# Kernel optimization log

Measured on AMD Instinct MI355X. Metric: run time of the kernel, lower is better.

The kernel has to match this reference:

```python
import jax, jax.numpy as jnp
import numpy as np

GAMMA, RHO, OMEGA = 0.7, 2.0, 0.5
EPS = 1e-6


def setup_inputs() -> dict:
    key = jax.random.key(0)
    S, T, N = 64, 256, 1024
    ks = jax.random.split(key, 7)
    x0 = jax.random.normal(ks[0], (N, 1), dtype=jnp.float32)
    # strictly increasing interaction times so dt > 0
    t = jnp.cumsum(jax.random.uniform(ks[1], (S, T), dtype=jnp.float32) + 0.1, axis=1)
    speed = jax.random.uniform(ks[2], (S, 1, 1, 1), dtype=jnp.float32) + 0.1
    vola = jax.random.uniform(ks[3], (S, 1, 1, 1), dtype=jnp.float32) + 0.1
    adj = (jax.random.uniform(ks[4], (N, N)) < 32.0 / N).astype(jnp.float32)
    noise = jax.random.normal(ks[5], (S, T - 1, N, 1), dtype=jnp.float32)
    items = jax.random.randint(ks[6], (S, T), 0, N)
    return {"x0": x0, "t": t, "speed": speed, "vola": vola,
            "adj": adj, "noise": noise, "items": items}


def _simulate(x0, t, speed, vola, adj, noise, items):
    S, T = t.shape
    N = x0.shape[0]
    dt = jnp.diff(t, axis=1)[:, :, None, None]                     # [S,T-1,1,1]
    # OU std: sqrt(vola^2 * (1 - exp(-2*speed*dt)) / (2*speed + 1e-6))
    scale = jnp.sqrt(vola * vola * (1.0 - jnp.exp(-2.0 * speed * dt))
                     / (2.0 * speed + 1e-6))                       # [S,T-1,1,1]
    noisy = noise * scale                                          # [S,T-1,N,1]

    adj_t = adj.T
    in_deg = adj_t.sum(axis=1)[None, :, None]                      # [1,N,1]
    has_in = in_deg > 0

    seq = jnp.arange(S)
    feat0 = jnp.zeros((S, N, 3), jnp.float32)
    feat0 = feat0.at[seq, items[:, 0], 0].add(1.0)
    feat0 = feat0.at[seq, items[:, 0], 2].add(1.0)
    x_init = jnp.broadcast_to(x0[None], (S, N, 1)).astype(jnp.float32)
    sp = speed[:, 0]                                               # [S,1,1]

    def step(carry, inp):
        x_prev, feat = carry
        dt_i, noisy_i, item_i = inp                                # [S,1,1],[S,N,1],[S]
        agg = jnp.einsum('mn,snk->smk', adj_t, x_prev)             # neighbor sum
        empower = jnp.where(has_in, GAMMA * agg / (in_deg + 1e-7), 0.0)
        stable = (feat[..., 1:2] / (feat[..., 0:1] + EPS)) ** RHO
        level = OMEGA * empower + (1.0 - OMEGA) * stable
        e = jnp.exp(-sp * dt_i)
        x_i = x_prev * e + (1.0 - e) * level + noisy_i
        cur_perf = jax.nn.sigmoid(x_i[seq, item_i, 0])
        success = (cur_perf >= 0.5).astype(jnp.float32)
        feat = feat.at[seq, item_i, 0].add(1.0)
        feat = feat.at[seq, item_i, 1].add(success)
        return (x_i, feat), x_i

    xs = (jnp.moveaxis(dt, 1, 0), jnp.moveaxis(noisy, 1, 0), items[:, 1:].T)
    (_, _), ys = jax.lax.scan(step, (x_init, feat0), xs)
    x = jnp.concatenate([x_init[:, None], jnp.moveaxis(ys, 0, 1)], axis=1)  # [S,T,N,1]
    return x


def reference(x0, t, speed, vola, adj, noise, items):
    return _simulate(x0, t, speed, vola, adj, noise, items)
```

## Files before the change

kernel.cpp:

```cpp
#include <hip/hip_runtime.h>

#define NN 1024
#define TT 256
#define MAXDEG 96

typedef unsigned short u16;
typedef unsigned long long ull;


__device__ __forceinline__ int bofsB(int v) {
    int h = (v >> 5) & 31;
    return 1024 + ((v & ~31) | ((v & 31) ^ h));
}
__device__ __forceinline__ int bofsC(int v) {
    int h = (v >> 5) & 31;
    return 2048 + ((v & ~31) | ((v & 31) ^ ((13 * h + 5) & 31)));
}
__device__ __forceinline__ int cnt_res(int pd, int res) {
    return (pd > res) ? (((pd - 1 - res) >> 5) + 1) : 0;
}
__device__ __forceinline__ int pd_of(int deg) {
    int cap = deg < MAXDEG ? deg : MAXDEG;
    int pd = (cap + 15) & ~7;
    if (pd < 16) pd = 16;
    if (pd > MAXDEG) pd = MAXDEG;
    return pd;
}

__global__ __launch_bounds__(64) void k1_count(const float* __restrict__ adj,
                                               int* __restrict__ cnt_part)
{
    int tid = blockIdx.x * 64 + threadIdx.x;
    int chunk = tid >> 10;
    int n = tid & 1023;
    int c = 0;
    for (int j = 0; j < 64; ++j)
        c += (adj[(chunk * 64 + j) * NN + n] != 0.0f) ? 1 : 0;
    cnt_part[chunk * NN + n] = c;
}

__global__ __launch_bounds__(1024) void k23_rank(const int* __restrict__ cnt_part,
                                                 int* __restrict__ deg,
                                                 int* __restrict__ rank_of,
                                                 int* __restrict__ node_of)
{
    __shared__ int pd_s[NN];
    const int n = threadIdx.x;
    int tot = 0;
    for (int c = 0; c < 16; ++c) tot += cnt_part[c * NN + n];
    deg[n] = tot;
    int my = pd_of(tot);
    pd_s[n] = my;
    __syncthreads();
    int r = 0;
    for (int m = 0; m < NN; ++m) {
        int pm = pd_s[m];
        r += (pm > my) || (pm == my && m < n);
    }
    rank_of[n] = r;
    node_of[r] = n;
}

__global__ __launch_bounds__(64) void k4_fill(const float* __restrict__ adj,
                                              const int* __restrict__ cnt_part,
                                              u16* __restrict__ nbrC)
{
    int tid = blockIdx.x * 64 + threadIdx.x;
    int chunk = tid >> 10;
    int n = tid & 1023;
    int pos = 0;
    for (int c = 0; c < chunk; ++c) pos += cnt_part[c * NN + n];
    for (int j = 0; j < 64; ++j) {
        int m = chunk * 64 + j;
        if (adj[m * NN + n] != 0.0f) {
            if (pos < MAXDEG) nbrC[n * MAXDEG + pos] = (u16)m;
            ++pos;
        }
    }
}

__global__ __launch_bounds__(64) void k5_sched(const u16* __restrict__ nbrC,
                                               const int* __restrict__ deg,
                                               const int* __restrict__ rank_of,
                                               u16* __restrict__ nbr8,
                                               int* __restrict__ ngrp_r,
                                               float* __restrict__ invd_r)
{
    const int tl = threadIdx.x;
    const int n  = blockIdx.x * 64 + tl;
    const int r  = rank_of[n];
    const int l  = r & 63;
    const int dg = deg[n];
    const int cap = dg < MAXDEG ? dg : MAXDEG;
    const int pd = pd_of(dg);

    ull freep = 0;
    for (int res = 0; res < 32; ++res)
        freep |= (ull)cnt_res(pd, res) << (2 * res);

    for (int g = 0; g < (pd >> 3); ++g) {
        uint4 pk;
        unsigned w0 = (unsigned)((3072 + ((l + g * 8 + 0) & 31)) * 4);
        unsigned w1 = (unsigned)((3072 + ((l + g * 8 + 1) & 31)) * 4);
        unsigned w2 = (unsigned)((3072 + ((l + g * 8 + 2) & 31)) * 4);
        unsigned w3 = (unsigned)((3072 + ((l + g * 8 + 3) & 31)) * 4);
        unsigned w4 = (unsigned)((3072 + ((l + g * 8 + 4) & 31)) * 4);
        unsigned w5 = (unsigned)((3072 + ((l + g * 8 + 5) & 31)) * 4);
        unsigned w6 = (unsigned)((3072 + ((l + g * 8 + 6) & 31)) * 4);
        unsigned w7 = (unsigned)((3072 + ((l + g * 8 + 7) & 31)) * 4);
        pk.x = w0 | (w1 << 16);
        pk.y = w2 | (w3 << 16);
        pk.z = w4 | (w5 << 16);
        pk.w = w6 | (w7 << 16);
        *(uint4*)(nbr8 + (g << 13) + (r << 3)) = pk;
    }

    const uint4* __restrict__ row = (const uint4*)(nbrC + n * MAXDEG);
    int maxk = 15;

    for (int c8 = 0; c8 < (cap + 7) / 8; ++c8) {
        uint4 w = row[c8];
        int id[8];
        id[0] = w.x & 0xFFFF; id[1] = w.x >> 16;
        id[2] = w.y & 0xFFFF; id[3] = w.y >> 16;
        id[4] = w.z & 0xFFFF; id[5] = w.z >> 16;
        id[6] = w.w & 0xFFFF; id[7] = w.w >> 16;
        int rk[8];
        #pragma unroll
        for (int u = 0; u < 8; ++u)
            rk[u] = rank_of[id[u]];

        int lim = cap - c8 * 8; if (lim > 8) lim = 8;
        #pragma unroll
        for (int u = 0; u < 8; ++u) {
            if (u >= lim) break;
            int v = rk[u];
            int b0 = v & 31;
            int h  = (v >> 5) & 31;
            int b1 = b0 ^ h;
            int b2 = b0 ^ ((13 * h + 5) & 31);
            int res0 = (b0 - l) & 31;
            int res1 = (b1 - l) & 31;
            int res2 = (b2 - l) & 31;
            int f0 = (int)((freep >> (2 * res0)) & 3);
            int f1 = (int)((freep >> (2 * res1)) & 3);
            int f2 = (int)((freep >> (2 * res2)) & 3);
            int kslot = -1, word = v, resw = 0, fw = 0;
            if (f0 > 0 && f0 >= f1 && f0 >= f2) {
                resw = res0; fw = f0; word = v;
            } else if (f1 > 0 && f1 >= f2) {
                resw = res1; fw = f1; word = bofsB(v);
            } else if (f2 > 0) {
                resw = res2; fw = f2; word = bofsC(v);
            } else {
                for (int res = 0; res < 32; ++res) {
                    int f = (int)((freep >> (2 * res)) & 3);
                    if (f > 0) { resw = res; fw = f; word = v; break; }
                }
            }
            if (fw > 0) {
                kslot = resw + 32 * (cnt_res(pd, resw) - fw);
                freep -= 1ull << (2 * resw);
                nbr8[((kslot >> 3) << 13) + (r << 3) + (kslot & 7)] = (u16)(word * 4);
                if (kslot > maxk) maxk = kslot;
            }
        }
    }
    ngrp_r[r] = (maxk >> 3) + 1;
    invd_r[r] = 0.35f / ((float)dg + 1e-7f);
}

#define LDS_BARRIER() asm volatile("s_waitcnt lgkmcnt(0)\n\ts_barrier" ::: "memory")

__global__ __launch_bounds__(1024) void sim_kernel(
    const float* __restrict__ x0, const float* __restrict__ t,
    const float* __restrict__ speed, const float* __restrict__ vola,
    const float* __restrict__ noise, const int* __restrict__ items,
    const u16* __restrict__ nbr8, const int* __restrict__ node_of,
    const int* __restrict__ rank_of,
    const int* __restrict__ ngrp_r, const float* __restrict__ invd_r,
    float* __restrict__ out)
{
    __shared__ float xb[2][3104];
    __shared__ float4 cst[TT - 1];

    const int s   = blockIdx.x;
    const int tid = threadIdx.x;

    const float sp = speed[s];
    const float vo = vola[s];

    if (tid < TT - 1) {
        float t0 = t[s * TT + tid], t1 = t[s * TT + tid + 1];
        float dt = t1 - t0;
        float e  = expf(-sp * dt);
        float sc = vo * sqrtf((1.0f - e * e) / (2.0f * sp + 1e-6f));
        int   it = items[s * TT + tid + 1];
        cst[tid] = make_float4(e, sc, __int_as_float(it), 0.0f);
    }

    const int   m     = node_of[tid];
    const int   r_out = rank_of[tid];
    const int   wB    = bofsB(tid);
    const int   wC    = bofsC(tid);

    const float x0m = x0[m];
    xb[0][tid] = x0m;
    xb[0][wB]  = x0m;
    xb[0][wC]  = x0m;
    if (tid < 32) { xb[0][3072 + tid] = 0.0f; xb[1][3072 + tid] = 0.0f; }

    float* __restrict__ outp = out + (size_t)s * TT * NN + tid;
    outp[0] = x0[tid];

    const int   ng   = ngrp_r[tid];
    const float invd = invd_r[tid];
    const int   item0 = items[s * TT];
    float a_f = (m == item0) ? 1.0f : 0.0f;
    float s_f = 0.0f;

    const float* __restrict__ nzm = noise + (size_t)s * (TT - 1) * NN + m;
    float nzA = nzm[0];
    float nzB = nzm[NN];

    const uint4* __restrict__ nb = (const uint4*)nbr8 + tid;
    uint4 q0  = nb[0];
    uint4 q1  = nb[1024];
    uint4 q2  = nb[2048];
    uint4 q3  = nb[3072];
    uint4 q4  = nb[4096];
    uint4 q5  = nb[5120];
    uint4 q6  = nb[6144];
    uint4 q7  = nb[7168];
    uint4 q8  = nb[8192];
    uint4 q9  = nb[9216];
    uint4 q10 = nb[10240];
    uint4 q11 = nb[11264];

    __syncthreads();

    float x_own = x0m;

#define G8(V)                                                   \
    acc += *(const float*)(xc + ((V).x & 0xFFFFu));             \
    acc += *(const float*)(xc + ((V).x >> 16));                 \
    acc += *(const float*)(xc + ((V).y & 0xFFFFu));             \
    acc += *(const float*)(xc + ((V).y >> 16));                 \
    acc += *(const float*)(xc + ((V).z & 0xFFFFu));             \
    acc += *(const float*)(xc + ((V).z >> 16));                 \
    acc += *(const float*)(xc + ((V).w & 0xFFFFu));             \
    acc += *(const float*)(xc + ((V).w >> 16));

    for (int i = 0; i < TT - 1; ++i) {
        const float* __restrict__ src = xb[i & 1];
        float* __restrict__ dst       = xb[(i + 1) & 1];
        const float4 c = cst[i];

        int ipre = (i + 2 < TT - 1) ? (i + 2) : (TT - 2);
        float nz_new = nzm[(size_t)ipre * NN];

        float xi_lin = src[r_out];

        float acc = 0.0f;
        const char* xc = (const char*)src;
        G8(q0); G8(q1);
        if (ng > 2) { G8(q2);
        if (ng > 3) { G8(q3);
        if (ng > 4) { G8(q4);
        if (ng > 5) { G8(q5);
        if (ng > 6) { G8(q6);
        if (ng > 7) { G8(q7);
        if (ng > 8) { G8(q8);
        if (ng > 9) { G8(q9);
        if (ng > 10){ G8(q10);
        if (ng > 11){ G8(q11); } } } } } } } } } }

        float nz = nzA * c.y;
        float r  = s_f / (a_f + 1e-6f);
        float level = fmaf(acc, invd, 0.5f * r * r);
        float xn = fmaf(x_own, c.x, fmaf(1.0f - c.x, level, nz));

        dst[tid] = xn;
        dst[wB]  = xn;
        dst[wC]  = xn;
        if (i) outp[(size_t)i * NN] = xi_lin;

        if (m == __float_as_int(c.z)) {
            a_f += 1.0f;
            s_f += (xn >= 0.0f) ? 1.0f : 0.0f;
        }
        x_own = xn;
        nzA = nzB; nzB = nz_new;
        LDS_BARRIER();
    }
#undef G8

    outp[(size_t)(TT - 1) * NN] = xb[1][r_out];
}

extern "C" void kernel_launch(void* const* d_in, const int* in_sizes, int n_in,
                              void* d_out, int out_size, void* d_ws, size_t ws_size,
                              hipStream_t stream)
{
    const float* x0    = (const float*)d_in[0];
    const float* t     = (const float*)d_in[1];
    const float* speed = (const float*)d_in[2];
    const float* vola  = (const float*)d_in[3];
    const float* adj   = (const float*)d_in[4];
    const float* noise = (const float*)d_in[5];
    const int*   items = (const int*)d_in[6];
    float* out = (float*)d_out;

    char* ws = (char*)d_ws;
    int*   cnt_part = (int*)ws;
    int*   deg      = (int*)(ws + 65536);
    int*   rank_of  = (int*)(ws + 65536 + 4096);
    int*   node_of  = (int*)(ws + 65536 + 8192);
    int*   ngrp_r   = (int*)(ws + 65536 + 12288);
    float* invd_r   = (float*)(ws + 65536 + 16384);
    u16*   nbrC     = (u16*)(ws + 65536 + 20480);
    u16*   nbr8     = (u16*)(ws + 65536 + 20480 + 196608);

    k1_count<<<256, 64, 0, stream>>>(adj, cnt_part);
    k23_rank<<<1, 1024, 0, stream>>>(cnt_part, deg, rank_of, node_of);
    k4_fill<<<256, 64, 0, stream>>>(adj, cnt_part, nbrC);
    k5_sched<<<16, 64, 0, stream>>>(nbrC, deg, rank_of, nbr8, ngrp_r, invd_r);
    sim_kernel<<<64, 1024, 0, stream>>>(x0, t, speed, vola, noise, items,
                                        nbr8, node_of, rank_of, ngrp_r, invd_r, out);
}
```

Baseline: 421.5 us.

## Fuse count and fill preprocessing kernels and add swap-based bank-conflict slot repair

Merges the degree-count and neighbor-fill passes into one kernel that keeps per-chunk counts in shared memory. This removes one launch and the global partial-count buffer. The scheduler also gains a repair step: when a neighbor's preferred bank-residue slots are full, it tries to move an already placed neighbor to one of that neighbor's alternate copies, rather than dropping to any free slot. That should cut LDS bank conflicts in the simulation gather, at the cost of more complex preprocessing and extra shared memory in the scheduler.

```diff
diff --git a/kernel.cpp b/kernel.cpp
--- a/kernel.cpp
+++ b/kernel.cpp
@@ -27,29 +27,41 @@
     return pd;
 }
 
-__global__ __launch_bounds__(64) void k1_count(const float* __restrict__ adj,
-                                               int* __restrict__ cnt_part)
-{
-    int tid = blockIdx.x * 64 + threadIdx.x;
-    int chunk = tid >> 10;
-    int n = tid & 1023;
+__global__ __launch_bounds__(1024) void p1_fill(const float* __restrict__ adj,
+                                                u16* __restrict__ nbrC,
+                                                int* __restrict__ deg)
+{
+    __shared__ int cnt_s[16][65];
+    const int nl = threadIdx.x & 63;
+    const int ch = threadIdx.x >> 6;
+    const int n  = blockIdx.x * 64 + nl;
+
     int c = 0;
     for (int j = 0; j < 64; ++j)
-        c += (adj[(chunk * 64 + j) * NN + n] != 0.0f) ? 1 : 0;
-    cnt_part[chunk * NN + n] = c;
-}
-
-__global__ __launch_bounds__(1024) void k23_rank(const int* __restrict__ cnt_part,
-                                                 int* __restrict__ deg,
-                                                 int* __restrict__ rank_of,
-                                                 int* __restrict__ node_of)
+        c += (adj[(ch * 64 + j) * NN + n] != 0.0f) ? 1 : 0;
+    cnt_s[ch][nl] = c;
+    __syncthreads();
+
+    int pos = 0;
+    for (int cc = 0; cc < ch; ++cc) pos += cnt_s[cc][nl];
+    if (ch == 15) deg[n] = pos + c;
+
+    for (int j = 0; j < 64; ++j) {
+        int mrow = ch * 64 + j;
+        if (adj[mrow * NN + n] != 0.0f) {
+            if (pos < MAXDEG) nbrC[n * MAXDEG + pos] = (u16)mrow;
+            ++pos;
+        }
+    }
+}
+
+__global__ __launch_bounds__(1024) void p2_rank(const int* __restrict__ deg,
+                                                int* __restrict__ rank_of,
+                                                int* __restrict__ node_of)
 {
     __shared__ int pd_s[NN];
     const int n = threadIdx.x;
-    int tot = 0;
-    for (int c = 0; c < 16; ++c) tot += cnt_part[c * NN + n];
-    deg[n] = tot;
-    int my = pd_of(tot);
+    int my = pd_of(deg[n]);
     pd_s[n] = my;
     __syncthreads();
     int r = 0;
@@ -61,31 +73,14 @@
     node_of[r] = n;
 }
 
-__global__ __launch_bounds__(64) void k4_fill(const float* __restrict__ adj,
-                                              const int* __restrict__ cnt_part,
-                                              u16* __restrict__ nbrC)
-{
-    int tid = blockIdx.x * 64 + threadIdx.x;
-    int chunk = tid >> 10;
-    int n = tid & 1023;
-    int pos = 0;
-    for (int c = 0; c < chunk; ++c) pos += cnt_part[c * NN + n];
-    for (int j = 0; j < 64; ++j) {
-        int m = chunk * 64 + j;
-        if (adj[m * NN + n] != 0.0f) {
-            if (pos < MAXDEG) nbrC[n * MAXDEG + pos] = (u16)m;
-            ++pos;
-        }
-    }
-}
-
-__global__ __launch_bounds__(64) void k5_sched(const u16* __restrict__ nbrC,
+__global__ __launch_bounds__(64) void p3_sched(const u16* __restrict__ nbrC,
                                                const int* __restrict__ deg,
                                                const int* __restrict__ rank_of,
                                                u16* __restrict__ nbr8,
                                                int* __restrict__ ngrp_r,
                                                float* __restrict__ invd_r)
 {
+    __shared__ u16 who_s[MAXDEG][64];
     const int tl = threadIdx.x;
     const int n  = blockIdx.x * 64 + tl;
     const int r  = rank_of[n];
@@ -97,6 +92,7 @@
     ull freep = 0;
     for (int res = 0; res < 32; ++res)
         freep |= (ull)cnt_res(pd, res) << (2 * res);
+    for (int k = 0; k < pd; ++k) who_s[k][tl] = 0xFFFF;
 
     for (int g = 0; g < (pd >> 3); ++g) {
         uint4 pk;
@@ -118,6 +114,8 @@
     const uint4* __restrict__ row = (const uint4*)(nbrC + n * MAXDEG);
     int maxk = 15;
 
+#define EMIT(K, WORD) nbr8[(((K) >> 3) << 13) + (r << 3) + ((K) & 7)] = (u16)((WORD) * 4)
+
     for (int c8 = 0; c8 < (cap + 7) / 8; ++c8) {
         uint4 w = row[c8];
         int id[8];
@@ -137,15 +135,13 @@
             int v = rk[u];
             int b0 = v & 31;
             int h  = (v >> 5) & 31;
-            int b1 = b0 ^ h;
-            int b2 = b0 ^ ((13 * h + 5) & 31);
             int res0 = (b0 - l) & 31;
-            int res1 = (b1 - l) & 31;
-            int res2 = (b2 - l) & 31;
+            int res1 = ((b0 ^ h) - l) & 31;
+            int res2 = ((b0 ^ ((13 * h + 5) & 31)) - l) & 31;
             int f0 = (int)((freep >> (2 * res0)) & 3);
             int f1 = (int)((freep >> (2 * res1)) & 3);
             int f2 = (int)((freep >> (2 * res2)) & 3);
-            int kslot = -1, word = v, resw = 0, fw = 0;
+            int resw, fw, word;
             if (f0 > 0 && f0 >= f1 && f0 >= f2) {
                 resw = res0; fw = f0; word = v;
             } else if (f1 > 0 && f1 >= f2) {
@@ -153,19 +149,63 @@
             } else if (f2 > 0) {
                 resw = res2; fw = f2; word = bofsC(v);
             } else {
-                for (int res = 0; res < 32; ++res) {
-                    int f = (int)((freep >> (2 * res)) & 3);
-                    if (f > 0) { resw = res; fw = f; word = v; break; }
+                fw = 0; resw = 0; word = v;
+            }
+            if (fw > 0) {
+                int kslot = resw + 32 * (cnt_res(pd, resw) - fw);
+                freep -= 1ull << (2 * resw);
+                EMIT(kslot, word);
+                who_s[kslot][tl] = (u16)v;
+                if (kslot > maxk) maxk = kslot;
+            } else {
+                int done = 0;
+                int rs[3] = {res0, res1, res2};
+                for (int ci = 0; ci < 3 && !done; ++ci) {
+                    int rc = rs[ci];
+                    int cnt = cnt_res(pd, rc);
+                    for (int p = 0; p < cnt && !done; ++p) {
+                        int k1 = rc + 32 * p;
+                        int vo = who_s[k1][tl];
+                        if (vo == 0xFFFF) continue;
+                        int ob0 = vo & 31;
+                        int oh  = (vo >> 5) & 31;
+                        int obs[3] = {ob0, ob0 ^ oh, ob0 ^ ((13 * oh + 5) & 31)};
+                        for (int oi = 0; oi < 3 && !done; ++oi) {
+                            int ro = (obs[oi] - l) & 31;
+                            int fo = (int)((freep >> (2 * ro)) & 3);
+                            if (fo > 0) {
+                                int k2 = ro + 32 * (cnt_res(pd, ro) - fo);
+                                freep -= 1ull << (2 * ro);
+                                int ow = (oi == 0) ? vo : (oi == 1) ? bofsB(vo) : bofsC(vo);
+                                EMIT(k2, ow);
+                                who_s[k2][tl] = (u16)vo;
+                                if (k2 > maxk) maxk = k2;
+                                int vw = (ci == 0) ? v : (ci == 1) ? bofsB(v) : bofsC(v);
+                                EMIT(k1, vw);
+                                who_s[k1][tl] = (u16)v;
+                                if (k1 > maxk) maxk = k1;
+                                done = 1;
+                            }
+                        }
+                    }
+                }
+                if (!done) {
+                    for (int res = 0; res < 32; ++res) {
+                        int f = (int)((freep >> (2 * res)) & 3);
+                        if (f > 0) {
+                            int kslot = res + 32 * (cnt_res(pd, res) - f);
+                            freep -= 1ull << (2 * res);
+                            EMIT(kslot, v);
+                            who_s[kslot][tl] = (u16)v;
+                            if (kslot > maxk) maxk = kslot;
+                            break;
+                        }
+                    }
                 }
             }
-            if (fw > 0) {
-                kslot = resw + 32 * (cnt_res(pd, resw) - fw);
-                freep -= 1ull << (2 * resw);
-                nbr8[((kslot >> 3) << 13) + (r << 3) + (kslot & 7)] = (u16)(word * 4);
-                if (kslot > maxk) maxk = kslot;
-            }
         }
     }
+#undef EMIT
     ngrp_r[r] = (maxk >> 3) + 1;
     invd_r[r] = 0.35f / ((float)dg + 1e-7f);
 }
@@ -312,19 +352,17 @@
     float* out = (float*)d_out;
 
     char* ws = (char*)d_ws;
-    int*   cnt_part = (int*)ws;
-    int*   deg      = (int*)(ws + 65536);
-    int*   rank_of  = (int*)(ws + 65536 + 4096);
-    int*   node_of  = (int*)(ws + 65536 + 8192);
-    int*   ngrp_r   = (int*)(ws + 65536 + 12288);
-    float* invd_r   = (float*)(ws + 65536 + 16384);
-    u16*   nbrC     = (u16*)(ws + 65536 + 20480);
-    u16*   nbr8     = (u16*)(ws + 65536 + 20480 + 196608);
-
-    k1_count<<<256, 64, 0, stream>>>(adj, cnt_part);
-    k23_rank<<<1, 1024, 0, stream>>>(cnt_part, deg, rank_of, node_of);
-    k4_fill<<<256, 64, 0, stream>>>(adj, cnt_part, nbrC);
-    k5_sched<<<16, 64, 0, stream>>>(nbrC, deg, rank_of, nbr8, ngrp_r, invd_r);
+    int*   deg      = (int*)ws;
+    int*   rank_of  = (int*)(ws + 4096);
+    int*   node_of  = (int*)(ws + 8192);
+    int*   ngrp_r   = (int*)(ws + 12288);
+    float* invd_r   = (float*)(ws + 16384);
+    u16*   nbrC     = (u16*)(ws + 20480);
+    u16*   nbr8     = (u16*)(ws + 20480 + 196608);
+
+    p1_fill<<<16, 1024, 0, stream>>>(adj, nbrC, deg);
+    p2_rank<<<1, 1024, 0, stream>>>(deg, rank_of, node_of);
+    p3_sched<<<16, 64, 0, stream>>>(nbrC, deg, rank_of, nbr8, ngrp_r, invd_r);
     sim_kernel<<<64, 1024, 0, stream>>>(x0, t, speed, vola, noise, items,
                                         nbr8, node_of, rank_of, ngrp_r, invd_r, out);
 }
```

After: 433.8 us. 2.9% more time.
